# Performance work log

Hardware: AMD Instinct MI355X
Metric: run time of the kernel (lower is better)

The kernel has to match this reference:

```python
import jax, jax.numpy as jnp
import numpy as np

DIM = 32      # feature dim (must be small: unnormalized det prod overflows fp32 otherwise)
K = 16        # number of mixture components / experts
B = 262144    # batch


def setup_inputs() -> dict:
    key = jax.random.key(0)
    k0, k1, k2, k3, k4 = jax.random.split(key, 5)
    x = jax.random.normal(k0, (B, DIM), dtype=jnp.float32)
    xavier = 1.0 / np.sqrt(DIM / 2.0)
    mu = (jax.random.normal(k1, (K, DIM), dtype=jnp.float32) * xavier)
    # torch init is ones; use small values so prod(2*pi*sigma2) stays finite in fp32
    logsigma = jax.random.normal(k2, (K, DIM), dtype=jnp.float32) * 0.1
    W = jax.random.normal(k3, (K, DIM, DIM), dtype=jnp.float32) * (1.0 / np.sqrt(DIM))
    b = jax.random.normal(k4, (K, DIM), dtype=jnp.float32) * 0.01
    return {"x": x, "mu": mu, "logsigma": logsigma, "W": W, "b": b}


def reference(x, mu, logsigma, W, b):
    # Gaussian prior pdf per expert, vectorized over k
    two_pi = np.float32(2.0 * np.pi)
    sigma2 = jnp.exp(2.0 * logsigma)                                   # [k, d]
    const = jax.lax.rsqrt(jnp.prod(two_pi * sigma2, axis=-1))           # [k]
    diff = x[None, :, :] - mu[:, None, :]                               # [k, b, d]
    exponent = -0.5 * jnp.sum(diff * diff / sigma2[:, None, :], axis=-1)  # [k, b]
    ps = const[:, None] * jnp.exp(exponent)                             # [k, b]
    w = ps / jnp.sum(ps, axis=0, keepdims=True)                         # [k, b]
    # per-expert Linear (torch convention: x @ W_k.T + b_k) + ReLU
    lik = jax.nn.relu(jnp.einsum('bd,kod->kbo', x, W) + b[:, None, :])  # [k, b, d]
    # gate-weighted sum over experts
    return jnp.einsum('kb,kbo->bo', w, lik)                             # [b, d]
```

## Files before the change

kernel.cpp:

```cpp
#include <hip/hip_runtime.h>
#include <math.h>

#define DIM 32
#define NK  16
#define LOG2E 1.4426950408889634f

typedef __attribute__((ext_vector_type(8))) short bf16x8;
typedef __attribute__((ext_vector_type(4))) float f32x4;

#define MFMA16 __builtin_amdgcn_mfma_f32_16x16x32_bf16

#define WHI_OFF 0
#define WLO_OFF 32768
#define HH_OFF  65536
#define HL_OFF  66560
#define GH_OFF  67584
#define GL_OFF  68608
#define CG_OFF  69632

__device__ __forceinline__ void split2(float x, short* hi, short* lo) {
  unsigned u = __float_as_uint(x);
  *hi = (short)(u >> 16);
  float hf = __uint_as_float(u & 0xFFFF0000u);
  float l = x - hf;
  *lo = (short)(__float_as_uint(l) >> 16);
}

__global__ __launch_bounds__(256) void gmm_setup_kernel(
    const float* __restrict__ mu, const float* __restrict__ logsigma,
    const float* __restrict__ W, char* __restrict__ ws)
{
  int i = blockIdx.x * 256 + threadIdx.x;
  short* whi = (short*)(ws + WHI_OFF);
  short* wlo = (short*)(ws + WLO_OFF);
  if (i < NK * DIM * DIM) split2(W[i], &whi[i], &wlo[i]);
  if (i < NK * DIM) {
    float s2 = __expf(2.0f * logsigma[i]);
    float h = (-0.5f / s2) * LOG2E;
    float g = (mu[i] / s2) * LOG2E;
    short a, b;
    split2(h, &a, &b);
    ((short*)(ws + HH_OFF))[i] = a; ((short*)(ws + HL_OFF))[i] = b;
    split2(g, &a, &b);
    ((short*)(ws + GH_OFF))[i] = a; ((short*)(ws + GL_OFF))[i] = b;
  }
  if (i < NK) {
    float acc = 0.0f;
    for (int d = 0; d < DIM; ++d) {
      float s2 = __expf(2.0f * logsigma[i * DIM + d]);
      float m  = mu[i * DIM + d];
      acc += m * m * (-0.5f / s2) * LOG2E - 0.5f * log2f(6.283185307179586f * s2);
    }
    ((float*)(ws + CG_OFF))[i] = acc;
  }
}

__global__ __launch_bounds__(256, 4) void gmm_moe_kernel(
    const float* __restrict__ x,
    const float* __restrict__ bias,
    const char* __restrict__ ws,
    float* __restrict__ out)
{
  __shared__ float lds_p[4][4][NK][16];
  const int wid  = threadIdx.x >> 6;
  const int lane = threadIdx.x & 63;
  const int g = lane >> 4;
  const int c = lane & 15;
  const int sbase = (blockIdx.x * 4 + wid) * 64;

  const bf16x8* whi = (const bf16x8*)(ws + WHI_OFF);
  const bf16x8* wlo = (const bf16x8*)(ws + WLO_OFF);
  const bf16x8 fhh = ((const bf16x8*)(ws + HH_OFF))[c * 4 + g];
  const bf16x8 fhl = ((const bf16x8*)(ws + HL_OFF))[c * 4 + g];
  const bf16x8 fgh = ((const bf16x8*)(ws + GH_OFF))[c * 4 + g];
  const bf16x8 fgl = ((const bf16x8*)(ws + GL_OFF))[c * 4 + g];
  const float  cgv = ((const float*)(ws + CG_OFF))[c];

  bf16x8 xh[4], xl[4];

  #pragma unroll
  for (int t = 0; t < 4; ++t) {
    const float* xp = x + (size_t)(sbase + t * 16 + c) * DIM + g * 8;
    float4 a0 = ((const float4*)xp)[0];
    float4 a1 = ((const float4*)xp)[1];
    float xv[8] = {a0.x, a0.y, a0.z, a0.w, a1.x, a1.y, a1.z, a1.w};
    bf16x8 x2h, x2l;
    #pragma unroll
    for (int j = 0; j < 8; ++j) {
      short h_, l_;
      split2(xv[j], &h_, &l_);
      xh[t][j] = h_; xl[t][j] = l_;
      float q = xv[j] * xv[j];
      split2(q, &h_, &l_);
      x2h[j] = h_; x2l[j] = l_;
    }
    f32x4 e = {cgv, cgv, cgv, cgv};
    e = MFMA16(x2h,   fhh, e, 0, 0, 0);
    e = MFMA16(x2l,   fhh, e, 0, 0, 0);
    e = MFMA16(x2h,   fhl, e, 0, 0, 0);
    e = MFMA16(xh[t], fgh, e, 0, 0, 0);
    e = MFMA16(xl[t], fgh, e, 0, 0, 0);
    e = MFMA16(xh[t], fgl, e, 0, 0, 0);
    float pr[4], sr[4];
    #pragma unroll
    for (int r = 0; r < 4; ++r) {
      pr[r] = __builtin_amdgcn_exp2f(e[r]);
      float s = pr[r];
      s += __shfl_xor(s, 1, 64);
      s += __shfl_xor(s, 2, 64);
      s += __shfl_xor(s, 4, 64);
      s += __shfl_xor(s, 8, 64);
      sr[r] = s;
    }
    f32x4 wv;
    #pragma unroll
    for (int r = 0; r < 4; ++r) wv[r] = pr[r] * __builtin_amdgcn_rcpf(sr[r]);
    *(f32x4*)&lds_p[wid][t][c][g * 4] = wv;
  }

  f32x4 o0[4], o1[4];
  #pragma unroll
  for (int t = 0; t < 4; ++t) { o0[t] = (f32x4){0,0,0,0}; o1[t] = (f32x4){0,0,0,0}; }

  for (int k = 0; k < NK; ++k) {
    bf16x8 w0h = whi[(k * DIM +      c) * 4 + g];
    bf16x8 w0l = wlo[(k * DIM +      c) * 4 + g];
    bf16x8 w1h = whi[(k * DIM + 16 + c) * 4 + g];
    bf16x8 w1l = wlo[(k * DIM + 16 + c) * 4 + g];
    float b0 = bias[k * DIM + c];
    float b1 = bias[k * DIM + 16 + c];
    #pragma unroll
    for (int t = 0; t < 4; ++t) {
      f32x4 s0 = {b0, b0, b0, b0}, s1 = {b1, b1, b1, b1};
      s0 = MFMA16(xh[t], w0h, s0, 0, 0, 0);
      s0 = MFMA16(xl[t], w0h, s0, 0, 0, 0);
      s0 = MFMA16(xh[t], w0l, s0, 0, 0, 0);
      s1 = MFMA16(xh[t], w1h, s1, 0, 0, 0);
      s1 = MFMA16(xl[t], w1h, s1, 0, 0, 0);
      s1 = MFMA16(xh[t], w1l, s1, 0, 0, 0);
      f32x4 wv = *(const f32x4*)&lds_p[wid][t][k][g * 4];
      #pragma unroll
      for (int r = 0; r < 4; ++r) {
        o0[t][r] = fmaf(wv[r], fmaxf(s0[r], 0.0f), o0[t][r]);
        o1[t][r] = fmaf(wv[r], fmaxf(s1[r], 0.0f), o1[t][r]);
      }
    }
  }

  #pragma unroll
  for (int t = 0; t < 4; ++t) {
    #pragma unroll
    for (int r = 0; r < 4; ++r) {
      size_t row = (size_t)(sbase + t * 16 + g * 4 + r);
      out[row * DIM + c]      = o0[t][r];
      out[row * DIM + 16 + c] = o1[t][r];
    }
  }
}

extern "C" void kernel_launch(void* const* d_in, const int* in_sizes, int n_in,
                              void* d_out, int out_size, void* d_ws, size_t ws_size,
                              hipStream_t stream) {
  const float* x  = (const float*)d_in[0];
  const float* mu = (const float*)d_in[1];
  const float* ls = (const float*)d_in[2];
  const float* W  = (const float*)d_in[3];
  const float* bv = (const float*)d_in[4];
  float* out = (float*)d_out;
  const int B = in_sizes[0] / DIM;

  gmm_setup_kernel<<<(NK * DIM * DIM + 255) / 256, 256, 0, stream>>>(
      mu, ls, W, (char*)d_ws);
  gmm_moe_kernel<<<B / 256, 256, 0, stream>>>(x, bv, (const char*)d_ws, out);
}
```

Before: 116.1 us.

## Stage W hi-part in LDS via async global_load_lds and hoist x loads

Each block now copies the 32 KB bf16 high half of W into LDS with asynchronous global-to-LDS loads, issued alongside the gating computation, and reads it from LDS in the expert loop. The low half still comes from global memory. The x loads are hoisted ahead of the setup loads, the expert loop is fully unrolled, and the ReLU-FMA accumulate uses vector builtins. The extra 32 KB of LDS per block and the looser launch bound (3 instead of 4) lower occupancy and add a block-wide barrier.

After: 114.9 us. Within noise of the previous version (-1.0%).

```diff
diff --git a/kernel.cpp b/kernel.cpp
--- a/kernel.cpp
+++ b/kernel.cpp
@@ -17,6 +17,9 @@
 #define GH_OFF  67584
 #define GL_OFF  68608
 #define CG_OFF  69632
+
+typedef __attribute__((address_space(1))) const unsigned int gu32;
+typedef __attribute__((address_space(3))) unsigned int lu32;
 
 __device__ __forceinline__ void split2(float x, short* hi, short* lo) {
   unsigned u = __float_as_uint(x);
@@ -55,35 +58,49 @@
   }
 }
 
-__global__ __launch_bounds__(256, 4) void gmm_moe_kernel(
+__global__ __launch_bounds__(256, 3) void gmm_moe_kernel(
     const float* __restrict__ x,
     const float* __restrict__ bias,
     const char* __restrict__ ws,
     float* __restrict__ out)
 {
+  __shared__ char  lds_w[32768];
   __shared__ float lds_p[4][4][NK][16];
-  const int wid  = threadIdx.x >> 6;
-  const int lane = threadIdx.x & 63;
+  const int tid  = threadIdx.x;
+  const int wid  = tid >> 6;
+  const int lane = tid & 63;
   const int g = lane >> 4;
   const int c = lane & 15;
   const int sbase = (blockIdx.x * 4 + wid) * 64;
 
-  const bf16x8* whi = (const bf16x8*)(ws + WHI_OFF);
-  const bf16x8* wlo = (const bf16x8*)(ws + WLO_OFF);
+  float4 xa[4][2];
+  #pragma unroll
+  for (int t = 0; t < 4; ++t) {
+    const float4* xp =
+        (const float4*)(x + (size_t)(sbase + t * 16 + c) * DIM + g * 8);
+    xa[t][0] = xp[0];
+    xa[t][1] = xp[1];
+  }
+
   const bf16x8 fhh = ((const bf16x8*)(ws + HH_OFF))[c * 4 + g];
   const bf16x8 fhl = ((const bf16x8*)(ws + HL_OFF))[c * 4 + g];
   const bf16x8 fgh = ((const bf16x8*)(ws + GH_OFF))[c * 4 + g];
   const bf16x8 fgl = ((const bf16x8*)(ws + GL_OFF))[c * 4 + g];
   const float  cgv = ((const float*)(ws + CG_OFF))[c];
 
+  #pragma unroll
+  for (int i = 0; i < 8; ++i) {
+    int off = wid * 8192 + i * 1024;
+    __builtin_amdgcn_global_load_lds(
+        (gu32*)(ws + WHI_OFF + off + lane * 16),
+        (lu32*)(lds_w + off), 16, 0, 0);
+  }
+
   bf16x8 xh[4], xl[4];
-
   #pragma unroll
   for (int t = 0; t < 4; ++t) {
-    const float* xp = x + (size_t)(sbase + t * 16 + c) * DIM + g * 8;
-    float4 a0 = ((const float4*)xp)[0];
-    float4 a1 = ((const float4*)xp)[1];
-    float xv[8] = {a0.x, a0.y, a0.z, a0.w, a1.x, a1.y, a1.z, a1.w};
+    float xv[8] = {xa[t][0].x, xa[t][0].y, xa[t][0].z, xa[t][0].w,
+                   xa[t][1].x, xa[t][1].y, xa[t][1].z, xa[t][1].w};
     bf16x8 x2h, x2l;
     #pragma unroll
     for (int j = 0; j < 8; ++j) {
@@ -118,17 +135,21 @@
     *(f32x4*)&lds_p[wid][t][c][g * 4] = wv;
   }
 
+  __syncthreads();
+
+  const bf16x8* wlo = (const bf16x8*)(ws + WLO_OFF);
   f32x4 o0[4], o1[4];
   #pragma unroll
   for (int t = 0; t < 4; ++t) { o0[t] = (f32x4){0,0,0,0}; o1[t] = (f32x4){0,0,0,0}; }
 
+  #pragma unroll
   for (int k = 0; k < NK; ++k) {
-    bf16x8 w0h = whi[(k * DIM +      c) * 4 + g];
-    bf16x8 w0l = wlo[(k * DIM +      c) * 4 + g];
-    bf16x8 w1h = whi[(k * DIM + 16 + c) * 4 + g];
-    bf16x8 w1l = wlo[(k * DIM + 16 + c) * 4 + g];
-    float b0 = bias[k * DIM + c];
-    float b1 = bias[k * DIM + 16 + c];
+    const bf16x8 w0h = *(const bf16x8*)(lds_w + k * 2048 + c * 64 + g * 16);
+    const bf16x8 w1h = *(const bf16x8*)(lds_w + k * 2048 + (16 + c) * 64 + g * 16);
+    const bf16x8 w0l = wlo[(k * DIM +      c) * 4 + g];
+    const bf16x8 w1l = wlo[(k * DIM + 16 + c) * 4 + g];
+    const float b0 = bias[k * DIM + c];
+    const float b1 = bias[k * DIM + 16 + c];
     #pragma unroll
     for (int t = 0; t < 4; ++t) {
       f32x4 s0 = {b0, b0, b0, b0}, s1 = {b1, b1, b1, b1};
@@ -138,12 +159,10 @@
       s1 = MFMA16(xh[t], w1h, s1, 0, 0, 0);
       s1 = MFMA16(xl[t], w1h, s1, 0, 0, 0);
       s1 = MFMA16(xh[t], w1l, s1, 0, 0, 0);
-      f32x4 wv = *(const f32x4*)&lds_p[wid][t][k][g * 4];
-      #pragma unroll
-      for (int r = 0; r < 4; ++r) {
-        o0[t][r] = fmaf(wv[r], fmaxf(s0[r], 0.0f), o0[t][r]);
-        o1[t][r] = fmaf(wv[r], fmaxf(s1[r], 0.0f), o1[t][r]);
-      }
+      const f32x4 wv = *(const f32x4*)&lds_p[wid][t][k][g * 4];
+      const f32x4 z = {0.0f, 0.0f, 0.0f, 0.0f};
+      o0[t] = __builtin_elementwise_fma(wv, __builtin_elementwise_max(s0, z), o0[t]);
+      o1[t] = __builtin_elementwise_fma(wv, __builtin_elementwise_max(s1, z), o1[t]);
     }
   }
 
```
